# Kernel tuning notes

Hardware: AMD Instinct MI355X
Metric: run time of the kernel (lower is better)

The kernel has to match this reference:

```python
import jax, jax.numpy as jnp
import numpy as np

EPS = 1e-08
STRIDE = 1


def setup_inputs() -> dict:
    key = jax.random.key(0)
    k_x, k_s, k_sw, k_w = jax.random.split(key, 4)
    B, Cin, Cout, D = 8, 32, 32, 48
    style_size, K = 2, 3
    x = jax.random.normal(k_x, (B, Cin, D, D, D), dtype=jnp.float32)
    s = jax.random.normal(k_s, (B, style_size), dtype=jnp.float32)
    # lecun_normal-style scaling for params
    style_weight = jax.random.normal(k_sw, (Cin, style_size), dtype=jnp.float32) / np.sqrt(style_size)
    style_bias = jnp.ones((Cin,), dtype=jnp.float32)
    weight = jax.random.normal(k_w, (Cout, Cin, K, K, K), dtype=jnp.float32) / np.sqrt(Cin * K * K * K)
    bias = jnp.zeros((Cout,), dtype=jnp.float32)
    return {"x": x, "s": s, "style_weight": style_weight,
            "style_bias": style_bias, "weight": weight, "bias": bias}


def reference(x, s, style_weight, style_bias, weight, bias):
    # Style modulation: per-sample per-input-channel scale  (B, Cin)
    s_mod = jnp.dot(s, style_weight.T) + style_bias
    # Modulated weights: (B, Cout, Cin, K, K, K)
    w = weight[None] * s_mod[:, None, :, None, None, None]
    # Demodulation over (Cin, K, K, K) per (B, Cout)
    norm = jnp.sqrt(jnp.sum(w ** 2, axis=(2, 3, 4, 5), keepdims=True) + jnp.float32(EPS))
    w_n = w / norm

    def single_conv(x_i, w_i):
        # x_i: (Cin, D, H, W), w_i: (Cout, Cin, K, K, K)
        out = jax.lax.conv_general_dilated(
            lhs=x_i[None], rhs=w_i,
            window_strides=(STRIDE,) * 3, padding='VALID',
            dimension_numbers=('NCDHW', 'OIDHW', 'NCDHW'))
        return out[0]

    y = jax.vmap(single_conv)(x, w_n)  # (B, Cout, D', H', W')
    return y + bias[None, :, None, None, None]
```

## Files before the change

### kernel.cpp

```cpp
#include <hip/hip_runtime.h>


typedef unsigned short u16;
typedef __bf16 bf16x8 __attribute__((ext_vector_type(8)));
typedef u16 u16x8 __attribute__((ext_vector_type(8)));
typedef float f32x4 __attribute__((ext_vector_type(4)));

#define CHUNKB   (110592 * 16)
#define XT_BYTES (32u * CHUNKB)
#define WA_ELEMS (8 * 4 * 32 * 28 * 8)

__device__ __forceinline__ u16 f2bf(float f) {
    __bf16 h = (__bf16)f;
    return __builtin_bit_cast(u16, h);
}

__device__ __forceinline__ void dma16(const void* g, void* l) {
    __builtin_amdgcn_global_load_lds(
        (const __attribute__((address_space(1))) unsigned*)g,
        (__attribute__((address_space(3))) unsigned*)l, 16, 0, 0);
}

__global__ __launch_bounds__(256) void xpose_kernel(
    const float* __restrict__ x, u16* __restrict__ xT)
{
    int gid = blockIdx.x * 256 + threadIdx.x;
    int quad = gid % 27648;
    int bc   = gid / 27648;
    int site0 = quad * 4;
    const float* xp = x + (size_t)bc * 8 * 110592 + site0;
    float4 v[8];
#pragma unroll
    for (int j = 0; j < 8; ++j) v[j] = *(const float4*)(xp + (size_t)j * 110592);
    u16* op = xT + (size_t)gid * 32;
#pragma unroll
    for (int k = 0; k < 4; ++k) {
        u16x8 o;
#pragma unroll
        for (int j = 0; j < 8; ++j) o[j] = f2bf(((const float*)&v[j])[k]);
        *(u16x8*)(op + k * 8) = o;
    }
}

__global__ __launch_bounds__(64) void wnorm8_kernel(
    const float* __restrict__ s, const float* __restrict__ sw,
    const float* __restrict__ sb, const float* __restrict__ w,
    u16* __restrict__ wA)
{
    int bc = blockIdx.x;
    int b = bc >> 5, co = bc & 31;
    int lane = threadIdx.x;
    float s0 = s[2 * b], s1 = s[2 * b + 1];

    float sum = 0.f;
    for (int i = lane; i < 864; i += 64) {
        int ci = i / 27;
        float m = fmaf(s0, sw[2 * ci], fmaf(s1, sw[2 * ci + 1], sb[ci]));
        float v = w[co * 864 + i] * m;
        sum += v * v;
    }
#pragma unroll
    for (int off = 32; off; off >>= 1) sum += __shfl_xor(sum, off, 64);
    float rn = 1.0f / sqrtf(sum + 1e-8f);

    for (int i = lane; i < 864; i += 64) {
        int ci = i / 27, tap = i - ci * 27;
        float m = fmaf(s0, sw[2 * ci], fmaf(s1, sw[2 * ci + 1], sb[ci]));
        float v = w[co * 864 + i] * m * rn;
        int chunk = ci >> 3, ci8 = ci & 7;
        wA[(((b * 4 + chunk) * 32 + co) * 28 + tap) * 8 + ci8] = f2bf(v);
    }
    if (lane < 32) {
        int c = lane >> 3, ci8 = lane & 7;
        wA[(((b * 4 + c) * 32 + co) * 28 + 27) * 8 + ci8] = 0;
    }
}

__global__ __launch_bounds__(512, 4) void conv_dma(
    const u16* __restrict__ xT, const u16* __restrict__ wA,
    const float* __restrict__ bias, float* __restrict__ out)
{
    __shared__ u16 sx[2][16384];

    int blk = blockIdx.x;
    int zt = blk % 12, yt = (blk / 12) % 12, b = blk / 144;
    int z0 = zt * 4, y0 = yt * 4;

    int t = threadIdx.x;
    int l = t & 63, w = t >> 6;
    int ln = l & 15;
    int tq = l >> 4;
    int zw = w & 3, yp = w >> 2;

    size_t goff[4];
#pragma unroll
    for (int i = 0; i < 4; ++i) {
        int sidx = t + i * 512;
        int z = sidx / 300, r = sidx - z * 300;
        int y = r / 50, x = r - y * 50;
        long o = ((long)((z0 + z) * 48 + (y0 + y)) * 48 + x) * 16;
        long mx = (long)CHUNKB - 16;
        goff[i] = (size_t)(o < mx ? o : mx);
    }

    int bbase[7];
#pragma unroll
    for (int s = 0; s < 7; ++s) {
        int tap = 4 * s + tq; if (tap > 26) tap = 26;
        int dz = tap / 9, rr = tap - dz * 9;
        int dy = rr / 3, dx = rr - dy * 3;
        bbase[s] = ((zw + dz) * 300 + (2 * yp + dy) * 50 + ln + dx) * 16;
    }
    int aoff = (ln * 28 + tq) * 16;

    f32x4 acc[2][3][2];
#pragma unroll
    for (int i = 0; i < 2; i++)
#pragma unroll
        for (int j = 0; j < 3; j++)
#pragma unroll
            for (int h = 0; h < 2; h++) acc[i][j][h] = (f32x4)0.f;

    const char* xc = (const char*)xT + (size_t)(b * 4) * CHUNKB;

#define ISSUE(c, d) { \
    _Pragma("unroll") \
    for (int i = 0; i < 4; ++i) \
        dma16(xc + (size_t)(c) * CHUNKB + goff[i], \
              (char*)&sx[d][0] + (size_t)(i * 512 + w * 64) * 16); }

#define COMPUTE(c, d) { \
    const char* wB = (const char*)(wA + (size_t)(b * 4 + (c)) * (32 * 28 * 8)); \
    const char* sb_ = (const char*)&sx[d][0]; \
    u16x8 A0 = *(const u16x8*)(wB + aoff); \
    u16x8 A1 = *(const u16x8*)(wB + aoff + 7168); \
    _Pragma("unroll") \
    for (int s = 0; s < 7; ++s) { \
        u16x8 nA0 = A0, nA1 = A1; \
        if (s < 6) { \
            nA0 = *(const u16x8*)(wB + aoff + (s + 1) * 64); \
            nA1 = *(const u16x8*)(wB + aoff + 7168 + (s + 1) * 64); \
        } \
        _Pragma("unroll") \
        for (int yr = 0; yr < 2; ++yr) { \
            const char* p = sb_ + bbase[s] + yr * 800; \
            _Pragma("unroll") \
            for (int xt = 0; xt < 3; ++xt) { \
                bf16x8 Bf = *(const bf16x8*)(p + xt * 256); \
                acc[yr][xt][0] = __builtin_amdgcn_mfma_f32_16x16x32_bf16( \
                    __builtin_bit_cast(bf16x8, A0), Bf, acc[yr][xt][0], 0, 0, 0); \
                acc[yr][xt][1] = __builtin_amdgcn_mfma_f32_16x16x32_bf16( \
                    __builtin_bit_cast(bf16x8, A1), Bf, acc[yr][xt][1], 0, 0, 0); \
            } \
        } \
        A0 = nA0; A1 = nA1; \
    } }

    ISSUE(0, 0)
    __syncthreads();
    ISSUE(1, 1)
    COMPUTE(0, 0)
    __syncthreads();
    ISSUE(2, 0)
    COMPUTE(1, 1)
    __syncthreads();
    ISSUE(3, 1)
    COMPUTE(2, 0)
    __syncthreads();
    COMPUTE(3, 1)

    int oz = z0 + zw;
    if (oz < 46) {
#pragma unroll
        for (int yr = 0; yr < 2; ++yr) {
            int oy = y0 + 2 * yp + yr;
            if (oy >= 46) continue;
#pragma unroll
            for (int xt = 0; xt < 3; ++xt) {
                int ox = xt * 16 + ln;
                if (ox >= 46) continue;
#pragma unroll
                for (int h = 0; h < 2; ++h) {
                    f32x4 a = acc[yr][xt][h];
#pragma unroll
                    for (int r = 0; r < 4; ++r) {
                        int co = h * 16 + tq * 4 + r;
                        out[(size_t)(b * 32 + co) * 97336 + oz * 2116 + oy * 46 + ox]
                            = a[r] + bias[co];
                    }
                }
            }
        }
    }
#undef ISSUE
#undef COMPUTE
}

__global__ __launch_bounds__(64) void wnorm16_kernel(
    const float* __restrict__ s, const float* __restrict__ sw,
    const float* __restrict__ sb, const float* __restrict__ w,
    u16* __restrict__ wA)
{
    int bc = blockIdx.x;
    int b = bc >> 5, co = bc & 31;
    int lane = threadIdx.x;
    float s0 = s[2 * b], s1 = s[2 * b + 1];

    float sum = 0.f;
    for (int i = lane; i < 864; i += 64) {
        int ci = i / 27;
        float m = fmaf(s0, sw[2 * ci], fmaf(s1, sw[2 * ci + 1], sb[ci]));
        float v = w[co * 864 + i] * m;
        sum += v * v;
    }
#pragma unroll
    for (int off = 32; off; off >>= 1) sum += __shfl_xor(sum, off, 64);
    float rn = 1.0f / sqrtf(sum + 1e-8f);

    for (int i = lane; i < 864; i += 64) {
        int ci = i / 27, tap = i - ci * 27;
        float m = fmaf(s0, sw[2 * ci], fmaf(s1, sw[2 * ci + 1], sb[ci]));
        float v = w[co * 864 + i] * m * rn;
        int chunk = ci >> 4, ci16 = ci & 15;
        wA[(((b * 2 + chunk) * 32 + co) * 28 + tap) * 16 + ci16] = f2bf(v);
    }
    if (lane < 32) {
        int c = lane >> 4, ci16 = lane & 15;
        wA[(((b * 2 + c) * 32 + co) * 28 + 27) * 16 + ci16] = 0;
    }
}

__global__ __launch_bounds__(512) void conv_fallback(
    const float* __restrict__ xin, const u16* __restrict__ wA,
    const float* __restrict__ bias, float* __restrict__ out)
{
    __shared__ u16 sx[28800];

    int blk = blockIdx.x;
    int zt = blk % 12, yt = (blk / 12) % 12, b = blk / 144;
    int z0 = zt * 4, y0 = yt * 4;

    int t = threadIdx.x;
    int l = t & 63, w = t >> 6;
    int ln = l & 15, ch = (l >> 4) & 1, tp = l >> 5, rg = l >> 4;
    int zw = w & 3, yp = w >> 2;

    f32x4 acc[2][3][2];
#pragma unroll
    for (int i = 0; i < 2; i++)
#pragma unroll
        for (int j = 0; j < 3; j++)
#pragma unroll
            for (int h = 0; h < 2; h++) acc[i][j][h] = (f32x4)0.f;

    for (int chunk = 0; chunk < 2; ++chunk) {
        __syncthreads();
        for (int idx = t; idx < 3600; idx += 512) {
            int x = idx % 50;
            int r = idx / 50;
            int cg = r & 1; r >>= 1;
            int y = r % 6, z = r / 6;
            int gz = z0 + z, gy = y0 + y;
            bool inb = (x < 48) && (gy < 48) && (gz < 48);
            const float* xp = xin + (size_t)(b * 32 + chunk * 16 + cg * 8) * 110592
                              + gz * 2304 + gy * 48 + x;
            u16x8 v;
#pragma unroll
            for (int j = 0; j < 8; j++) {
                float f = inb ? xp[(size_t)j * 110592] : 0.f;
                v[j] = f2bf(f);
            }
            *(u16x8*)&sx[idx * 8] = v;
        }
        __syncthreads();

        const u16* wAc = wA + (b * 2 + chunk) * (32 * 28 * 16);
        int aoff = (ln * 28 + tp) * 16 + ch * 8;

#pragma unroll
        for (int s = 0; s < 14; ++s) {
            int tapA = 2 * s + tp;
            bf16x8 A0 = __builtin_bit_cast(bf16x8, *(const u16x8*)(wAc + aoff + s * 32));
            bf16x8 A1 = __builtin_bit_cast(bf16x8, *(const u16x8*)(wAc + aoff + 16 * 28 * 16 + s * 32));
            int tapB = tapA > 26 ? 26 : tapA;
            int dz = tapB / 9;
            int rr = tapB - dz * 9;
            int dy = rr / 3;
            int dx = rr - dy * 3;
            int zr = zw + dz;
#pragma unroll
            for (int yr = 0; yr < 2; ++yr) {
                int yy = 2 * yp + yr + dy;
                int eb = (((zr * 6 + yy) * 2 + ch) * 50 + ln + dx) * 8;
#pragma unroll
                for (int xt = 0; xt < 3; ++xt) {
                    bf16x8 Bf = __builtin_bit_cast(bf16x8, *(const u16x8*)&sx[eb + xt * 128]);
                    acc[yr][xt][0] = __builtin_amdgcn_mfma_f32_16x16x32_bf16(A0, Bf, acc[yr][xt][0], 0, 0, 0);
                    acc[yr][xt][1] = __builtin_amdgcn_mfma_f32_16x16x32_bf16(A1, Bf, acc[yr][xt][1], 0, 0, 0);
                }
            }
        }
    }

    int oz = z0 + zw;
    if (oz < 46) {
#pragma unroll
        for (int yr = 0; yr < 2; ++yr) {
            int oy = y0 + 2 * yp + yr;
            if (oy >= 46) continue;
#pragma unroll
            for (int xt = 0; xt < 3; ++xt) {
                int ox = xt * 16 + ln;
                if (ox >= 46) continue;
#pragma unroll
                for (int h = 0; h < 2; ++h) {
                    f32x4 a = acc[yr][xt][h];
#pragma unroll
                    for (int r = 0; r < 4; ++r) {
                        int co = h * 16 + rg * 4 + r;
                        out[(size_t)(b * 32 + co) * 97336 + oz * 2116 + oy * 46 + ox]
                            = a[r] + bias[co];
                    }
                }
            }
        }
    }
}

extern "C" void kernel_launch(void* const* d_in, const int* in_sizes, int n_in,
                              void* d_out, int out_size, void* d_ws, size_t ws_size,
                              hipStream_t stream) {
    const float* x    = (const float*)d_in[0];
    const float* s    = (const float*)d_in[1];
    const float* sw   = (const float*)d_in[2];
    const float* sb   = (const float*)d_in[3];
    const float* wgt  = (const float*)d_in[4];
    const float* bias = (const float*)d_in[5];
    float* out = (float*)d_out;

    const size_t need = (size_t)XT_BYTES + WA_ELEMS * sizeof(u16);
    if (ws_size >= need) {
        u16* xT = (u16*)d_ws;
        u16* wA = (u16*)((char*)d_ws + XT_BYTES);
        hipLaunchKernelGGL(xpose_kernel, dim3(3456), dim3(256), 0, stream, x, xT);
        hipLaunchKernelGGL(wnorm8_kernel, dim3(256), dim3(64), 0, stream,
                           s, sw, sb, wgt, wA);
        hipLaunchKernelGGL(conv_dma, dim3(12 * 12 * 8), dim3(512), 0, stream,
                           xT, wA, bias, out);
    } else {
        u16* wA = (u16*)d_ws;
        hipLaunchKernelGGL(wnorm16_kernel, dim3(256), dim3(64), 0, stream,
                           s, sw, sb, wgt, wA);
        hipLaunchKernelGGL(conv_fallback, dim3(12 * 12 * 8), dim3(512), 0, stream,
                           x, wA, bias, out);
    }
}
```

Before: 112.7 us.

## Halve conv tile height to shrink LDS and raise occupancy

Each conv block now covers 4 z by 2 y output rows instead of 4 by 4. That halves the accumulators per wave, cuts the LDS slab from 6x6x50 to 6x4x50 voxels per chunk, and doubles the grid to 2208 blocks. Launch bounds request 8 waves-per-EU residency instead of 4. The aim is better occupancy and latency hiding, at the cost of more halo reloading (4 input rows loaded per 2 output rows) and less weight-fragment reuse per LDS read.

```diff
diff --git a/kernel.cpp b/kernel.cpp
--- a/kernel.cpp
+++ b/kernel.cpp
@@ -76,15 +76,15 @@
     }
 }
 
-__global__ __launch_bounds__(512, 4) void conv_dma(
+__global__ __launch_bounds__(512, 8) void conv_dma(
     const u16* __restrict__ xT, const u16* __restrict__ wA,
     const float* __restrict__ bias, float* __restrict__ out)
 {
-    __shared__ u16 sx[2][16384];
+    __shared__ u16 sx[2][9728];
 
     int blk = blockIdx.x;
-    int zt = blk % 12, yt = (blk / 12) % 12, b = blk / 144;
-    int z0 = zt * 4, y0 = yt * 4;
+    int zt = blk % 12, yt = (blk / 12) % 23, b = blk / 276;
+    int z0 = zt * 4, y0 = yt * 2;
 
     int t = threadIdx.x;
     int l = t & 63, w = t >> 6;
@@ -92,42 +92,35 @@
     int tq = l >> 4;
     int zw = w & 3, yp = w >> 2;
 
-    size_t goff[4];
-#pragma unroll
-    for (int i = 0; i < 4; ++i) {
-        int sidx = t + i * 512;
-        int z = sidx / 300, r = sidx - z * 300;
-        int y = r / 50, x = r - y * 50;
-        long o = ((long)((z0 + z) * 48 + (y0 + y)) * 48 + x) * 16;
-        long mx = (long)CHUNKB - 16;
-        goff[i] = (size_t)(o < mx ? o : mx);
-    }
-
     int bbase[7];
 #pragma unroll
     for (int s = 0; s < 7; ++s) {
         int tap = 4 * s + tq; if (tap > 26) tap = 26;
         int dz = tap / 9, rr = tap - dz * 9;
         int dy = rr / 3, dx = rr - dy * 3;
-        bbase[s] = ((zw + dz) * 300 + (2 * yp + dy) * 50 + ln + dx) * 16;
+        bbase[s] = ((zw + dz) * 200 + (yp + dy) * 50 + ln + dx) * 16;
     }
     int aoff = (ln * 28 + tq) * 16;
 
-    f32x4 acc[2][3][2];
-#pragma unroll
-    for (int i = 0; i < 2; i++)
-#pragma unroll
-        for (int j = 0; j < 3; j++)
-#pragma unroll
-            for (int h = 0; h < 2; h++) acc[i][j][h] = (f32x4)0.f;
+    f32x4 acc[3][2];
+#pragma unroll
+    for (int j = 0; j < 3; j++)
+#pragma unroll
+        for (int h = 0; h < 2; h++) acc[j][h] = (f32x4)0.f;
 
     const char* xc = (const char*)xT + (size_t)(b * 4) * CHUNKB;
 
-#define ISSUE(c, d) { \
-    _Pragma("unroll") \
-    for (int i = 0; i < 4; ++i) \
-        dma16(xc + (size_t)(c) * CHUNKB + goff[i], \
-              (char*)&sx[d][0] + (size_t)(i * 512 + w * 64) * 16); }
+#define ISSUE1(c, d, i, cond) if (cond) { \
+    int sidx = t + (i) * 512; \
+    int z = sidx / 200, r_ = sidx - z * 200; \
+    int y = r_ / 50, x = r_ - y * 50; \
+    long o = ((long)((z0 + z) * 48 + (y0 + y)) * 48 + x) * 16; \
+    long mx = (long)CHUNKB - 16; \
+    size_t go = (size_t)(o < mx ? o : mx); \
+    dma16(xc + (size_t)(c) * CHUNKB + go, \
+          (char*)&sx[d][0] + (size_t)((i) * 512 + w * 64) * 16); }
+
+#define ISSUE(c, d) ISSUE1(c, d, 0, true) ISSUE1(c, d, 1, true) ISSUE1(c, d, 2, (w < 3))
 
 #define COMPUTE(c, d) { \
     const char* wB = (const char*)(wA + (size_t)(b * 4 + (c)) * (32 * 28 * 8)); \
@@ -141,17 +134,14 @@
             nA0 = *(const u16x8*)(wB + aoff + (s + 1) * 64); \
             nA1 = *(const u16x8*)(wB + aoff + 7168 + (s + 1) * 64); \
         } \
+        const char* p = sb_ + bbase[s]; \
         _Pragma("unroll") \
-        for (int yr = 0; yr < 2; ++yr) { \
-            const char* p = sb_ + bbase[s] + yr * 800; \
-            _Pragma("unroll") \
-            for (int xt = 0; xt < 3; ++xt) { \
-                bf16x8 Bf = *(const bf16x8*)(p + xt * 256); \
-                acc[yr][xt][0] = __builtin_amdgcn_mfma_f32_16x16x32_bf16( \
-                    __builtin_bit_cast(bf16x8, A0), Bf, acc[yr][xt][0], 0, 0, 0); \
-                acc[yr][xt][1] = __builtin_amdgcn_mfma_f32_16x16x32_bf16( \
-                    __builtin_bit_cast(bf16x8, A1), Bf, acc[yr][xt][1], 0, 0, 0); \
-            } \
+        for (int xt = 0; xt < 3; ++xt) { \
+            bf16x8 Bf = *(const bf16x8*)(p + xt * 256); \
+            acc[xt][0] = __builtin_amdgcn_mfma_f32_16x16x32_bf16( \
+                __builtin_bit_cast(bf16x8, A0), Bf, acc[xt][0], 0, 0, 0); \
+            acc[xt][1] = __builtin_amdgcn_mfma_f32_16x16x32_bf16( \
+                __builtin_bit_cast(bf16x8, A1), Bf, acc[xt][1], 0, 0, 0); \
         } \
         A0 = nA0; A1 = nA1; \
     } }
@@ -170,29 +160,26 @@
     COMPUTE(3, 1)
 
     int oz = z0 + zw;
+    int oy = y0 + yp;
     if (oz < 46) {
 #pragma unroll
-        for (int yr = 0; yr < 2; ++yr) {
-            int oy = y0 + 2 * yp + yr;
-            if (oy >= 46) continue;
-#pragma unroll
-            for (int xt = 0; xt < 3; ++xt) {
-                int ox = xt * 16 + ln;
-                if (ox >= 46) continue;
-#pragma unroll
-                for (int h = 0; h < 2; ++h) {
-                    f32x4 a = acc[yr][xt][h];
-#pragma unroll
-                    for (int r = 0; r < 4; ++r) {
-                        int co = h * 16 + tq * 4 + r;
-                        out[(size_t)(b * 32 + co) * 97336 + oz * 2116 + oy * 46 + ox]
-                            = a[r] + bias[co];
-                    }
+        for (int xt = 0; xt < 3; ++xt) {
+            int ox = xt * 16 + ln;
+            if (ox >= 46) continue;
+#pragma unroll
+            for (int h = 0; h < 2; ++h) {
+                f32x4 a = acc[xt][h];
+#pragma unroll
+                for (int r = 0; r < 4; ++r) {
+                    int co = h * 16 + tq * 4 + r;
+                    out[(size_t)(b * 32 + co) * 97336 + oz * 2116 + oy * 46 + ox]
+                        = a[r] + bias[co];
                 }
             }
         }
     }
 #undef ISSUE
+#undef ISSUE1
 #undef COMPUTE
 }
 
@@ -345,7 +332,7 @@
         hipLaunchKernelGGL(xpose_kernel, dim3(3456), dim3(256), 0, stream, x, xT);
         hipLaunchKernelGGL(wnorm8_kernel, dim3(256), dim3(64), 0, stream,
                            s, sw, sb, wgt, wA);
-        hipLaunchKernelGGL(conv_dma, dim3(12 * 12 * 8), dim3(512), 0, stream,
+        hipLaunchKernelGGL(conv_dma, dim3(12 * 23 * 8), dim3(512), 0, stream,
                            xT, wA, bias, out);
     } else {
         u16* wA = (u16*)d_ws;
```

Measured after the change: 143.1 us. 1.27x slower.

## Load full 32-channel halo tile once and reduce over K=32 per tap

Applied to the files above, without the earlier changes.

The transposed activation layout becomes channel-last with all 32 input channels per site (four 8-channel groups), and the weights are repacked as [b][co][tap][ci] so each MFMA contracts over the 32 input channels of one tap. The conv kernel loads the whole 6x6x50 halo tile for a block into LDS in a single pass, with an XOR rotation of the channel groups to avoid bank conflicts. It then reuses each loaded B fragment across the three dy taps instead of running the previous 4-stage double-buffered chunk pipeline. Blocks are remapped so consecutive block IDs cover different batches. The trade-off is a much larger LDS footprint (about 115 KB), which drops occupancy and removes the overlap of loads with compute.

```diff
diff --git a/kernel.cpp b/kernel.cpp
--- a/kernel.cpp
+++ b/kernel.cpp
@@ -6,9 +6,8 @@
 typedef u16 u16x8 __attribute__((ext_vector_type(8)));
 typedef float f32x4 __attribute__((ext_vector_type(4)));
 
-#define CHUNKB   (110592 * 16)
-#define XT_BYTES (32u * CHUNKB)
-#define WA_ELEMS (8 * 4 * 32 * 28 * 8)
+#define XT_BYTES  (8u * 110592u * 32u * 2u)
+#define WA2_ELEMS (8 * 32 * 27 * 32)
 
 __device__ __forceinline__ u16 f2bf(float f) {
     __bf16 h = (__bf16)f;
@@ -25,27 +24,28 @@
     const float* __restrict__ x, u16* __restrict__ xT)
 {
     int gid = blockIdx.x * 256 + threadIdx.x;
-    int quad = gid % 27648;
-    int bc   = gid / 27648;
+    int cg   = gid & 3;
+    int tmp  = gid >> 2;
+    int quad = tmp % 27648;
+    int b    = tmp / 27648;
     int site0 = quad * 4;
-    const float* xp = x + (size_t)bc * 8 * 110592 + site0;
+    const float* xp = x + (size_t)(b * 32 + cg * 8) * 110592 + site0;
     float4 v[8];
 #pragma unroll
     for (int j = 0; j < 8; ++j) v[j] = *(const float4*)(xp + (size_t)j * 110592);
-    u16* op = xT + (size_t)gid * 32;
 #pragma unroll
     for (int k = 0; k < 4; ++k) {
         u16x8 o;
 #pragma unroll
         for (int j = 0; j < 8; ++j) o[j] = f2bf(((const float*)&v[j])[k]);
-        *(u16x8*)(op + k * 8) = o;
-    }
-}
-
-__global__ __launch_bounds__(64) void wnorm8_kernel(
+        *(u16x8*)(xT + ((size_t)(b * 110592 + site0 + k) * 4 + cg) * 8) = o;
+    }
+}
+
+__global__ __launch_bounds__(64) void wnorm32_kernel(
     const float* __restrict__ s, const float* __restrict__ sw,
     const float* __restrict__ sb, const float* __restrict__ w,
-    u16* __restrict__ wA)
+    u16* __restrict__ wA2)
 {
     int bc = blockIdx.x;
     int b = bc >> 5, co = bc & 31;
@@ -67,22 +67,19 @@
         int ci = i / 27, tap = i - ci * 27;
         float m = fmaf(s0, sw[2 * ci], fmaf(s1, sw[2 * ci + 1], sb[ci]));
         float v = w[co * 864 + i] * m * rn;
-        int chunk = ci >> 3, ci8 = ci & 7;
-        wA[(((b * 4 + chunk) * 32 + co) * 28 + tap) * 8 + ci8] = f2bf(v);
-    }
-    if (lane < 32) {
-        int c = lane >> 3, ci8 = lane & 7;
-        wA[(((b * 4 + c) * 32 + co) * 28 + 27) * 8 + ci8] = 0;
-    }
-}
-
-__global__ __launch_bounds__(512, 4) void conv_dma(
-    const u16* __restrict__ xT, const u16* __restrict__ wA,
+        wA2[((size_t)(b * 32 + co) * 27 + tap) * 32 + ci] = f2bf(v);
+    }
+}
+
+__global__ __launch_bounds__(512) void conv_one(
+    const u16* __restrict__ xT, const u16* __restrict__ wA2,
     const float* __restrict__ bias, float* __restrict__ out)
 {
-    __shared__ u16 sx[2][16384];
-
-    int blk = blockIdx.x;
+    __shared__ u16 sx[57600];
+
+    int orig = blockIdx.x;
+    int blk = (orig & 7) * 144 + (orig >> 3);
+
     int zt = blk % 12, yt = (blk / 12) % 12, b = blk / 144;
     int z0 = zt * 4, y0 = yt * 4;
 
@@ -90,28 +87,25 @@
     int l = t & 63, w = t >> 6;
     int ln = l & 15;
     int tq = l >> 4;
-    int zw = w & 3, yp = w >> 2;
-
-    size_t goff[4];
-#pragma unroll
-    for (int i = 0; i < 4; ++i) {
-        int sidx = t + i * 512;
-        int z = sidx / 300, r = sidx - z * 300;
-        int y = r / 50, x = r - y * 50;
-        long o = ((long)((z0 + z) * 48 + (y0 + y)) * 48 + x) * 16;
-        long mx = (long)CHUNKB - 16;
-        goff[i] = (size_t)(o < mx ? o : mx);
-    }
-
-    int bbase[7];
-#pragma unroll
-    for (int s = 0; s < 7; ++s) {
-        int tap = 4 * s + tq; if (tap > 26) tap = 26;
-        int dz = tap / 9, rr = tap - dz * 9;
-        int dy = rr / 3, dx = rr - dy * 3;
-        bbase[s] = ((zw + dz) * 300 + (2 * yp + dy) * 50 + ln + dx) * 16;
-    }
-    int aoff = (ln * 28 + tq) * 16;
+    int zw = w & 3, yp = (w >> 2) & 1;
+
+#pragma unroll
+    for (int i = 0; i < 15; ++i) {
+        int idx = i * 512 + t;
+        if (idx < 7200) {
+            int site = idx >> 2, slot = idx & 3;
+            int row = site / 50, x = site - row * 50;
+            int zp = row / 6, yq = row - zp * 6;
+            int gz = z0 + zp; if (gz > 47) gz = 47;
+            int gy = y0 + yq; if (gy > 47) gy = 47;
+            int gx = x > 47 ? 47 : x;
+            int rot = (row + (x >> 1)) & 3;
+            int g = slot ^ rot;
+            const u16* src = xT + ((size_t)(b * 110592 + (gz * 48 + gy) * 48 + gx) * 4 + g) * 8;
+            dma16(src, (char*)sx + (size_t)idx * 16);
+        }
+    }
+    __syncthreads();
 
     f32x4 acc[2][3][2];
 #pragma unroll
@@ -121,53 +115,48 @@
 #pragma unroll
             for (int h = 0; h < 2; h++) acc[i][j][h] = (f32x4)0.f;
 
-    const char* xc = (const char*)xT + (size_t)(b * 4) * CHUNKB;
-
-#define ISSUE(c, d) { \
-    _Pragma("unroll") \
-    for (int i = 0; i < 4; ++i) \
-        dma16(xc + (size_t)(c) * CHUNKB + goff[i], \
-              (char*)&sx[d][0] + (size_t)(i * 512 + w * 64) * 16); }
-
-#define COMPUTE(c, d) { \
-    const char* wB = (const char*)(wA + (size_t)(b * 4 + (c)) * (32 * 28 * 8)); \
-    const char* sb_ = (const char*)&sx[d][0]; \
-    u16x8 A0 = *(const u16x8*)(wB + aoff); \
-    u16x8 A1 = *(const u16x8*)(wB + aoff + 7168); \
-    _Pragma("unroll") \
-    for (int s = 0; s < 7; ++s) { \
-        u16x8 nA0 = A0, nA1 = A1; \
-        if (s < 6) { \
-            nA0 = *(const u16x8*)(wB + aoff + (s + 1) * 64); \
-            nA1 = *(const u16x8*)(wB + aoff + 7168 + (s + 1) * 64); \
-        } \
-        _Pragma("unroll") \
-        for (int yr = 0; yr < 2; ++yr) { \
-            const char* p = sb_ + bbase[s] + yr * 800; \
-            _Pragma("unroll") \
-            for (int xt = 0; xt < 3; ++xt) { \
-                bf16x8 Bf = *(const bf16x8*)(p + xt * 256); \
-                acc[yr][xt][0] = __builtin_amdgcn_mfma_f32_16x16x32_bf16( \
-                    __builtin_bit_cast(bf16x8, A0), Bf, acc[yr][xt][0], 0, 0, 0); \
-                acc[yr][xt][1] = __builtin_amdgcn_mfma_f32_16x16x32_bf16( \
-                    __builtin_bit_cast(bf16x8, A1), Bf, acc[yr][xt][1], 0, 0, 0); \
-            } \
-        } \
-        A0 = nA0; A1 = nA1; \
-    } }
-
-    ISSUE(0, 0)
-    __syncthreads();
-    ISSUE(1, 1)
-    COMPUTE(0, 0)
-    __syncthreads();
-    ISSUE(2, 0)
-    COMPUTE(1, 1)
-    __syncthreads();
-    ISSUE(3, 1)
-    COMPUTE(2, 0)
-    __syncthreads();
-    COMPUTE(3, 1)
+    const u16* wAb = wA2 + (size_t)(b * 32) * 27 * 32;
+
+#pragma unroll
+    for (int dz = 0; dz < 3; ++dz) {
+#pragma unroll
+        for (int dx = 0; dx < 3; ++dx) {
+            u16x8 Bf[4][3];
+#pragma unroll
+            for (int r = 0; r < 4; ++r) {
+                int rowi = (zw + dz) * 6 + 2 * yp + r;
+#pragma unroll
+                for (int xt = 0; xt < 3; ++xt) {
+                    int xx = xt * 16 + ln + dx;
+                    int site = rowi * 50 + xx;
+                    int rot = (rowi + ((ln + dx) >> 1)) & 3;
+                    int boff = site * 64 + ((tq ^ rot) << 4);
+                    Bf[r][xt] = *(const u16x8*)((const char*)sx + boff);
+                }
+            }
+            u16x8 Af[3][2];
+#pragma unroll
+            for (int dy = 0; dy < 3; ++dy) {
+                int tap = (dz * 3 + dy) * 3 + dx;
+#pragma unroll
+                for (int h = 0; h < 2; ++h)
+                    Af[dy][h] = *(const u16x8*)(wAb
+                        + ((size_t)(ln + 16 * h) * 27 + tap) * 32 + tq * 8);
+            }
+#pragma unroll
+            for (int dy = 0; dy < 3; ++dy)
+#pragma unroll
+                for (int yr = 0; yr < 2; ++yr)
+#pragma unroll
+                    for (int xt = 0; xt < 3; ++xt)
+#pragma unroll
+                        for (int h = 0; h < 2; ++h)
+                            acc[yr][xt][h] = __builtin_amdgcn_mfma_f32_16x16x32_bf16(
+                                __builtin_bit_cast(bf16x8, Af[dy][h]),
+                                __builtin_bit_cast(bf16x8, Bf[yr + dy][xt]),
+                                acc[yr][xt][h], 0, 0, 0);
+        }
+    }
 
     int oz = z0 + zw;
     if (oz < 46) {
@@ -192,8 +181,6 @@
             }
         }
     }
-#undef ISSUE
-#undef COMPUTE
 }
 
 __global__ __launch_bounds__(64) void wnorm16_kernel(
@@ -338,15 +325,15 @@
     const float* bias = (const float*)d_in[5];
     float* out = (float*)d_out;
 
-    const size_t need = (size_t)XT_BYTES + WA_ELEMS * sizeof(u16);
+    const size_t need = (size_t)XT_BYTES + WA2_ELEMS * sizeof(u16);
     if (ws_size >= need) {
-        u16* xT = (u16*)d_ws;
-        u16* wA = (u16*)((char*)d_ws + XT_BYTES);
+        u16* xT  = (u16*)d_ws;
+        u16* wA2 = (u16*)((char*)d_ws + XT_BYTES);
         hipLaunchKernelGGL(xpose_kernel, dim3(3456), dim3(256), 0, stream, x, xT);
-        hipLaunchKernelGGL(wnorm8_kernel, dim3(256), dim3(64), 0, stream,
-                           s, sw, sb, wgt, wA);
-        hipLaunchKernelGGL(conv_dma, dim3(12 * 12 * 8), dim3(512), 0, stream,
-                           xT, wA, bias, out);
+        hipLaunchKernelGGL(wnorm32_kernel, dim3(256), dim3(64), 0, stream,
+                           s, sw, sb, wgt, wA2);
+        hipLaunchKernelGGL(conv_one, dim3(12 * 12 * 8), dim3(512), 0, stream,
+                           xT, wA2, bias, out);
     } else {
         u16* wA = (u16*)d_ws;
         hipLaunchKernelGGL(wnorm16_kernel, dim3(256), dim3(64), 0, stream,
```

After: 112.4 us. About the same (-0.3%).
